# Kernel optimization log

Measured on AMD Instinct MI355X. Metric: run time of the kernel, lower is better.

The kernel has to match this reference:

```python
import jax, jax.numpy as jnp
import numpy as np

B, N, DIM = 4, 2048, 1024
HEAD = 16
INTER = 1024
HD = INTER // HEAD  # 64
SCALE = INTER ** (-0.5)


def setup_inputs() -> dict:
    key = jax.random.key(0)
    k1, k2, k3 = jax.random.split(key, 3)
    features = jax.random.normal(k1, (B, N, DIM), dtype=jnp.float32)
    W_qkv = jax.random.normal(k2, (DIM, 3 * INTER), dtype=jnp.float32) * (DIM ** -0.5)
    W_out = jax.random.normal(k3, (INTER, DIM), dtype=jnp.float32) * (INTER ** -0.5)
    return {"features": features, "W_qkv": W_qkv, "W_out": W_out}


def reference(features, W_qkv, W_out):
    # fc_qkv: [b, n, 3*inter], chunk into q, k, v
    qkv = jnp.einsum('bnd,de->bne', features, W_qkv)
    q, k, v = jnp.split(qkv, 3, axis=-1)
    # b n (h d) -> b n h d
    q = q.reshape(B, N, HEAD, HD)
    k = k.reshape(B, N, HEAD, HD)
    v = v.reshape(B, N, HEAD, HD)
    # scores: b h i j  (scale = inter_dim ** -0.5, as in source)
    alpha = jnp.einsum('bihd,bjhd->bhij', q, k) * SCALE
    att = jax.nn.softmax(alpha, axis=-1)
    out = jnp.einsum('bhij,bjhd->bihd', att, v)
    out = out.reshape(B, N, INTER)
    # fc_out (dropout_ratio=0.0 -> identity)
    return jnp.einsum('bni,id->bnd', out, W_out)
```

## Files before the change

kernel.cpp:

```cpp
#include <hip/hip_runtime.h>
#include <stdint.h>

#define BB 4
#define SEQ 2048
#define DMODEL 1024
#define NHEAD 16
#define HDIM 64
#define INTER 1024
#define QSCALE 0.045084220027780106f

#if __has_builtin(__builtin_amdgcn_exp2f)
#define EXP2F(x) __builtin_amdgcn_exp2f(x)
#else
#define EXP2F(x) exp2f(x)
#endif

typedef unsigned short u16;
typedef __attribute__((ext_vector_type(4))) unsigned short u16x4;
typedef __attribute__((ext_vector_type(4))) short s16x4;
typedef __attribute__((ext_vector_type(8))) short s16x8;
typedef __attribute__((ext_vector_type(4))) float f32x4;
typedef __attribute__((ext_vector_type(16))) float f32x16;

__device__ __forceinline__ u16 f2bf(float f) {
  unsigned int u = __float_as_uint(f);
  u += 0x7FFFu + ((u >> 16) & 1u);
  return (u16)(u >> 16);
}

#if __has_builtin(__builtin_amdgcn_cvt_pk_bf16_f32)
typedef __attribute__((ext_vector_type(2))) __bf16 bf16x2_t;
__device__ __forceinline__ unsigned int pk2bf(float a, float b) {
  bf16x2_t r = __builtin_amdgcn_cvt_pk_bf16_f32(a, b);
  return *reinterpret_cast<unsigned int*>(&r);
}
#else
__device__ __forceinline__ unsigned int pk2bf(float a, float b) {
  return (unsigned int)f2bf(a) | ((unsigned int)f2bf(b) << 16);
}
#endif

__device__ __forceinline__ void async16(const u16* g, u16* l) {
  __builtin_amdgcn_global_load_lds((__attribute__((address_space(1))) void*)(void*)(g),
                                   (__attribute__((address_space(3))) void*)(l),
                                   16, 0, 0);
}

__global__ __launch_bounds__(256) void prep(
    const float* __restrict__ f, const float* __restrict__ wqkv,
    const float* __restrict__ wout, u16* __restrict__ Xb,
    u16* __restrict__ WqkvT, u16* __restrict__ WoutT) {
  __shared__ float tile[32][33];
  const int bid = blockIdx.x, tid = threadIdx.x;
  if (bid < 8192) {
    int i = (bid * 256 + tid) * 4;
    f32x4 v = *reinterpret_cast<const f32x4*>(f + i);
    uint2 o;
    o.x = pk2bf(v[0], v[1]);
    o.y = pk2bf(v[2], v[3]);
    *reinterpret_cast<uint2*>(Xb + i) = o;
  } else {
    const float* src; u16* dst; int rows, cols, bx, by;
    if (bid < 8192 + 3072) {
      int t = bid - 8192;
      src = wqkv; dst = WqkvT; rows = DMODEL; cols = 3 * INTER;
      bx = t % 96; by = t / 96;
    } else {
      int t = bid - 11264;
      src = wout; dst = WoutT; rows = INTER; cols = DMODEL;
      bx = t & 31; by = t >> 5;
    }
    int c0 = bx * 32, r0 = by * 32, tx = tid & 31, ty = tid >> 5;
    #pragma unroll
    for (int i = ty; i < 32; i += 8) tile[i][tx] = src[(size_t)(r0 + i) * cols + c0 + tx];
    __syncthreads();
    #pragma unroll
    for (int i = ty; i < 32; i += 8)
      dst[(size_t)(c0 + i) * rows + r0 + tx] = f2bf(tile[tx][i]);
  }
}

template <int MODE>
__global__ __launch_bounds__(256, 2) void gemm_bt(
    const u16* __restrict__ A, const u16* __restrict__ BT,
    float* __restrict__ Cf, u16* __restrict__ Qb, u16* __restrict__ Kp,
    u16* __restrict__ Vp, int K, int ldc) {
  __shared__ u16 As[128 * 32];
  __shared__ u16 Bs[128 * 32];
  const int tid = threadIdx.x;
  const int wave = tid >> 6, lane = tid & 63;
  const int row0 = blockIdx.y * 128, col0 = blockIdx.x * 128;
  const int wr = (wave >> 1) * 64, wc = (wave & 1) * 64;
  const int r = lane & 15, q8 = (lane >> 4) * 8;

  f32x4 acc[4][4] = {};

  const int sRow = lane >> 2, sK = (lane & 3) * 8;
  const u16* Ag0 = A + (size_t)(row0 + wave * 32 + sRow) * K + sK;
  const u16* Ag1 = Ag0 + (size_t)16 * K;
  const u16* Bg0 = BT + (size_t)(col0 + wave * 32 + sRow) * K + sK;
  const u16* Bg1 = Bg0 + (size_t)16 * K;
  u16* Al0 = &As[wave * 1024];
  u16* Al1 = Al0 + 512;
  u16* Bl0 = &Bs[wave * 1024];
  u16* Bl1 = Bl0 + 512;

  for (int k0 = 0; k0 < K; k0 += 32) {
    async16(Ag0 + k0, Al0);
    async16(Ag1 + k0, Al1);
    async16(Bg0 + k0, Bl0);
    async16(Bg1 + k0, Bl1);
    __syncthreads();
    s16x8 af[4], bf[4];
    #pragma unroll
    for (int t = 0; t < 4; t++) {
      af[t] = *reinterpret_cast<const s16x8*>(&As[(wr + t * 16 + r) * 32 + q8]);
      bf[t] = *reinterpret_cast<const s16x8*>(&Bs[(wc + t * 16 + r) * 32 + q8]);
    }
    #pragma unroll
    for (int i = 0; i < 4; i++)
      #pragma unroll
      for (int j = 0; j < 4; j++)
        acc[i][j] = __builtin_amdgcn_mfma_f32_16x16x32_bf16(af[i], bf[j], acc[i][j], 0, 0, 0);
    __syncthreads();
  }

  const int quad = lane >> 4;
  #pragma unroll
  for (int i = 0; i < 4; i++) {
    const int n = row0 + wr + i * 16 + quad * 4;
    const int b = n >> 11, nn = n & (SEQ - 1);
    #pragma unroll
    for (int j = 0; j < 4; j++) {
      const int gc = col0 + wc + j * 16 + r;
      if (MODE == 1) {
        #pragma unroll
        for (int reg = 0; reg < 4; reg++)
          Cf[(size_t)(n + reg) * ldc + gc] = acc[i][j][reg];
      } else if (gc < INTER) {
        size_t base = (size_t)n * INTER + gc;
        #pragma unroll
        for (int reg = 0; reg < 4; reg++)
          Qb[base + (size_t)reg * INTER] = f2bf(acc[i][j][reg] * QSCALE);
      } else if (gc < 2 * INTER) {
        int dim = gc - INTER, h = dim >> 6, d = dim & 63;
        int bh = b * NHEAD + h;
        size_t base = (((size_t)(bh * 64 + (nn >> 5)) * 4 + (d >> 4)) * 64 +
                       ((((d >> 3) & 1) << 5) | (nn & 31))) * 8 + (d & 7);
        #pragma unroll
        for (int reg = 0; reg < 4; reg++)
          Kp[base + reg * 8] = f2bf(acc[i][j][reg]);
      } else {
        int dim = gc - 2 * INTER, h = dim >> 6, d = dim & 63;
        int bh = b * NHEAD + h;
        size_t base = ((((size_t)(bh * 64 + (nn >> 5)) * 2 + ((nn >> 4) & 1)) * 2 +
                        (d >> 5)) * 64 +
                       ((((nn >> 3) & 1) << 5) | (d & 31))) * 8 + (nn & 7);
        uint2 pk;
        pk.x = pk2bf(acc[i][j][0], acc[i][j][1]);
        pk.y = pk2bf(acc[i][j][2], acc[i][j][3]);
        *reinterpret_cast<uint2*>(Vp + base) = pk;
      }
    }
  }
}

#define ATTN_STEP(JCUR, KC, KN)                                                   \
  {                                                                               \
    const int jnext = ((JCUR) + 1) & 63;                                          \
    _Pragma("unroll")                                                             \
    for (int c = 0; c < 4; c++)                                                   \
      KN[c] = *reinterpret_cast<const s16x8*>(kpb + jnext * 2048 + c * 512);      \
    s16x8 vf[4];                                                                  \
    _Pragma("unroll")                                                             \
    for (int c = 0; c < 4; c++)                                                   \
      vf[c] = *reinterpret_cast<const s16x8*>(vpb + (JCUR) * 2048 + c * 512);     \
    f32x16 st = {};                                                               \
    _Pragma("unroll")                                                             \
    for (int c = 0; c < 4; c++)                                                   \
      st = __builtin_amdgcn_mfma_f32_32x32x16_bf16(KC[c], qf[c], st, 0, 0, 0);    \
    _Pragma("unroll")                                                             \
    for (int q = 0; q < 4; q++) {                                                 \
      float p0 = EXP2F(st[q * 4 + 0]), p1 = EXP2F(st[q * 4 + 1]);                 \
      float p2 = EXP2F(st[q * 4 + 2]), p3 = EXP2F(st[q * 4 + 3]);                 \
      ls += (p0 + p1) + (p2 + p3);                                                \
      uint2 pk;                                                                   \
      pk.x = pk2bf(p0, p1);                                                       \
      pk.y = pk2bf(p2, p3);                                                       \
      *reinterpret_cast<uint2*>(&Pw[l31 * 36 + q * 8 + half * 4]) = pk;           \
    }                                                                             \
    _Pragma("unroll")                                                             \
    for (int kc = 0; kc < 2; kc++) {                                              \
      const u16* pp = &Pw[l31 * 36 + half * 8 + kc * 16];                         \
      s16x4 plo = *reinterpret_cast<const s16x4*>(pp);                            \
      s16x4 phi = *reinterpret_cast<const s16x4*>(pp + 4);                        \
      s16x8 pb = __builtin_shufflevector(plo, phi, 0, 1, 2, 3, 4, 5, 6, 7);       \
      ot0 = __builtin_amdgcn_mfma_f32_32x32x16_bf16(vf[kc * 2 + 0], pb, ot0, 0, 0, 0); \
      ot1 = __builtin_amdgcn_mfma_f32_32x32x16_bf16(vf[kc * 2 + 1], pb, ot1, 0, 0, 0); \
    }                                                                             \
  }

__global__ __launch_bounds__(128, 4) void attn_kernel(
    const u16* __restrict__ Qb, const u16* __restrict__ Kp,
    const u16* __restrict__ Vp, u16* __restrict__ AO) {
  __shared__ __align__(16) u16 Ps[2][32 * 36];
  const int tid = threadIdx.x;
  const int wave = tid >> 6, lane = tid & 63;
  const int l31 = lane & 31, half = lane >> 5;
  const int bh = blockIdx.x, b = bh >> 4, h = bh & 15;
  const int i0 = blockIdx.y * 64 + wave * 32;

  const u16* qbase = Qb + (size_t)(b * SEQ + i0 + l31) * INTER + h * HDIM + half * 8;
  s16x8 qf[4];
  #pragma unroll
  for (int c = 0; c < 4; c++) qf[c] = *reinterpret_cast<const s16x8*>(qbase + c * 16);

  const u16* kpb = Kp + (size_t)bh * (64 * 4 * 512) + lane * 8;
  const u16* vpb = Vp + (size_t)bh * (64 * 4 * 512) + lane * 8;
  u16* Pw = &Ps[wave][0];

  f32x16 ot0 = {}, ot1 = {};
  float ls = 0.f;

  s16x8 kf0[4], kf1[4];
  #pragma unroll
  for (int c = 0; c < 4; c++)
    kf0[c] = *reinterpret_cast<const s16x8*>(kpb + c * 512);

  for (int jb = 0; jb < 64; jb += 2) {
    ATTN_STEP(jb, kf0, kf1)
    ATTN_STEP(jb + 1, kf1, kf0)
  }

  ls += __shfl_xor(ls, 32, 64);
  float rinv = 1.0f / ls;

  u16* orow = AO + (size_t)(b * SEQ + i0 + l31) * INTER + h * HDIM;
  #pragma unroll
  for (int dt = 0; dt < 2; dt++) {
    const f32x16& o = dt ? ot1 : ot0;
    #pragma unroll
    for (int q = 0; q < 4; q++) {
      uint2 pk;
      pk.x = pk2bf(o[q * 4 + 0] * rinv, o[q * 4 + 1] * rinv);
      pk.y = pk2bf(o[q * 4 + 2] * rinv, o[q * 4 + 3] * rinv);
      *reinterpret_cast<uint2*>(orow + dt * 32 + q * 8 + half * 4) = pk;
    }
  }
}

extern "C" void kernel_launch(void* const* d_in, const int* in_sizes, int n_in,
                              void* d_out, int out_size, void* d_ws, size_t ws_size,
                              hipStream_t stream) {
  const float* features = (const float*)d_in[0];
  const float* W_qkv    = (const float*)d_in[1];
  const float* W_out    = (const float*)d_in[2];
  float* out = (float*)d_out;
  char* w = (char*)d_ws;
  u16* Xb    = (u16*)(w);
  u16* WqkvT = (u16*)(w + 16777216);
  u16* WoutT = (u16*)(w + 23068672);
  u16* Qb    = (u16*)(w + 25165824);
  u16* Kp    = (u16*)(w + 41943040);
  u16* Vp    = (u16*)(w + 58720256);
  u16* AO    = (u16*)(w + 75497472);

  prep<<<dim3(12288), dim3(256), 0, stream>>>(features, W_qkv, W_out, Xb, WqkvT, WoutT);
  gemm_bt<0><<<dim3(24, 64), dim3(256), 0, stream>>>(Xb, WqkvT, nullptr, Qb, Kp, Vp,
                                                     DMODEL, 0);
  attn_kernel<<<dim3(64, 32), dim3(128), 0, stream>>>(Qb, Kp, Vp, AO);
  gemm_bt<1><<<dim3(8, 64), dim3(256), 0, stream>>>(AO, WoutT, out, nullptr, nullptr,
                                                    nullptr, INTER, DMODEL);
}
```

Measured before the change: 287.9 us.

## Replace LDS P transpose with permlane32 swaps, add MFMA priority and XCD-aware block mapping

```diff
diff --git a/kernel.cpp b/kernel.cpp
--- a/kernel.cpp
+++ b/kernel.cpp
@@ -21,6 +21,7 @@
 typedef __attribute__((ext_vector_type(8))) short s16x8;
 typedef __attribute__((ext_vector_type(4))) float f32x4;
 typedef __attribute__((ext_vector_type(16))) float f32x16;
+typedef __attribute__((ext_vector_type(4))) unsigned int u32x4;
 
 __device__ __forceinline__ u16 f2bf(float f) {
   unsigned int u = __float_as_uint(f);
@@ -44,6 +45,30 @@
   __builtin_amdgcn_global_load_lds((__attribute__((address_space(1))) void*)(void*)(g),
                                    (__attribute__((address_space(3))) void*)(l),
                                    16, 0, 0);
+}
+
+__device__ __forceinline__ void make_pb(const unsigned int* cc, int half,
+                                        s16x8& pb0, s16x8& pb1) {
+#if __has_builtin(__builtin_amdgcn_permlane32_swap)
+  (void)half;
+  auto r02 = __builtin_amdgcn_permlane32_swap(cc[0], cc[2], false, false);
+  auto r13 = __builtin_amdgcn_permlane32_swap(cc[1], cc[3], false, false);
+  auto r46 = __builtin_amdgcn_permlane32_swap(cc[4], cc[6], false, false);
+  auto r57 = __builtin_amdgcn_permlane32_swap(cc[5], cc[7], false, false);
+  u32x4 w0 = {(unsigned)r02[0], (unsigned)r13[0], (unsigned)r02[1], (unsigned)r13[1]};
+  u32x4 w1 = {(unsigned)r46[0], (unsigned)r57[0], (unsigned)r46[1], (unsigned)r57[1]};
+#else
+  unsigned x0 = __shfl_xor((int)cc[0], 32, 64), x1 = __shfl_xor((int)cc[1], 32, 64);
+  unsigned x2 = __shfl_xor((int)cc[2], 32, 64), x3 = __shfl_xor((int)cc[3], 32, 64);
+  unsigned x4 = __shfl_xor((int)cc[4], 32, 64), x5 = __shfl_xor((int)cc[5], 32, 64);
+  unsigned x6 = __shfl_xor((int)cc[6], 32, 64), x7 = __shfl_xor((int)cc[7], 32, 64);
+  u32x4 w0 = {half ? x2 : cc[0], half ? x3 : cc[1],
+              half ? cc[2] : x0, half ? cc[3] : x1};
+  u32x4 w1 = {half ? x6 : cc[4], half ? x7 : cc[5],
+              half ? cc[6] : x4, half ? cc[7] : x5};
+#endif
+  pb0 = *reinterpret_cast<s16x8*>(&w0);
+  pb1 = *reinterpret_cast<s16x8*>(&w1);
 }
 
 __global__ __launch_bounds__(256) void prep(
@@ -176,39 +201,42 @@
     for (int c = 0; c < 4; c++)                                                   \
       vf[c] = *reinterpret_cast<const s16x8*>(vpb + (JCUR) * 2048 + c * 512);     \
     f32x16 st = {};                                                               \
+    __builtin_amdgcn_s_setprio(1);                                                \
     _Pragma("unroll")                                                             \
     for (int c = 0; c < 4; c++)                                                   \
       st = __builtin_amdgcn_mfma_f32_32x32x16_bf16(KC[c], qf[c], st, 0, 0, 0);    \
+    __builtin_amdgcn_s_setprio(0);                                                \
+    unsigned int cc[8];                                                           \
     _Pragma("unroll")                                                             \
     for (int q = 0; q < 4; q++) {                                                 \
       float p0 = EXP2F(st[q * 4 + 0]), p1 = EXP2F(st[q * 4 + 1]);                 \
       float p2 = EXP2F(st[q * 4 + 2]), p3 = EXP2F(st[q * 4 + 3]);                 \
       ls += (p0 + p1) + (p2 + p3);                                                \
-      uint2 pk;                                                                   \
-      pk.x = pk2bf(p0, p1);                                                       \
-      pk.y = pk2bf(p2, p3);                                                       \
-      *reinterpret_cast<uint2*>(&Pw[l31 * 36 + q * 8 + half * 4]) = pk;           \
+      cc[q * 2 + 0] = pk2bf(p0, p1);                                              \
+      cc[q * 2 + 1] = pk2bf(p2, p3);                                              \
     }                                                                             \
-    _Pragma("unroll")                                                             \
-    for (int kc = 0; kc < 2; kc++) {                                              \
-      const u16* pp = &Pw[l31 * 36 + half * 8 + kc * 16];                         \
-      s16x4 plo = *reinterpret_cast<const s16x4*>(pp);                            \
-      s16x4 phi = *reinterpret_cast<const s16x4*>(pp + 4);                        \
-      s16x8 pb = __builtin_shufflevector(plo, phi, 0, 1, 2, 3, 4, 5, 6, 7);       \
-      ot0 = __builtin_amdgcn_mfma_f32_32x32x16_bf16(vf[kc * 2 + 0], pb, ot0, 0, 0, 0); \
-      ot1 = __builtin_amdgcn_mfma_f32_32x32x16_bf16(vf[kc * 2 + 1], pb, ot1, 0, 0, 0); \
-    }                                                                             \
+    s16x8 pb0, pb1;                                                               \
+    make_pb(cc, half, pb0, pb1);                                                  \
+    __builtin_amdgcn_s_setprio(1);                                                \
+    ot0 = __builtin_amdgcn_mfma_f32_32x32x16_bf16(vf[0], pb0, ot0, 0, 0, 0);      \
+    ot1 = __builtin_amdgcn_mfma_f32_32x32x16_bf16(vf[1], pb0, ot1, 0, 0, 0);      \
+    ot0 = __builtin_amdgcn_mfma_f32_32x32x16_bf16(vf[2], pb1, ot0, 0, 0, 0);      \
+    ot1 = __builtin_amdgcn_mfma_f32_32x32x16_bf16(vf[3], pb1, ot1, 0, 0, 0);      \
+    __builtin_amdgcn_s_setprio(0);                                                \
   }
 
 __global__ __launch_bounds__(128, 4) void attn_kernel(
     const u16* __restrict__ Qb, const u16* __restrict__ Kp,
     const u16* __restrict__ Vp, u16* __restrict__ AO) {
-  __shared__ __align__(16) u16 Ps[2][32 * 36];
   const int tid = threadIdx.x;
   const int wave = tid >> 6, lane = tid & 63;
   const int l31 = lane & 31, half = lane >> 5;
-  const int bh = blockIdx.x, b = bh >> 4, h = bh & 15;
-  const int i0 = blockIdx.y * 64 + wave * 32;
+  const int wg = blockIdx.x;
+  const int xcd = wg & 7, li = wg >> 3;
+  const int bh = xcd + ((li >> 5) << 3);
+  const int iblk = li & 31;
+  const int b = bh >> 4, h = bh & 15;
+  const int i0 = iblk * 64 + wave * 32;
 
   const u16* qbase = Qb + (size_t)(b * SEQ + i0 + l31) * INTER + h * HDIM + half * 8;
   s16x8 qf[4];
@@ -217,7 +245,6 @@
 
   const u16* kpb = Kp + (size_t)bh * (64 * 4 * 512) + lane * 8;
   const u16* vpb = Vp + (size_t)bh * (64 * 4 * 512) + lane * 8;
-  u16* Pw = &Ps[wave][0];
 
   f32x16 ot0 = {}, ot1 = {};
   float ls = 0.f;
@@ -268,7 +295,7 @@
   prep<<<dim3(12288), dim3(256), 0, stream>>>(features, W_qkv, W_out, Xb, WqkvT, WoutT);
   gemm_bt<0><<<dim3(24, 64), dim3(256), 0, stream>>>(Xb, WqkvT, nullptr, Qb, Kp, Vp,
                                                      DMODEL, 0);
-  attn_kernel<<<dim3(64, 32), dim3(128), 0, stream>>>(Qb, Kp, Vp, AO);
+  attn_kernel<<<dim3(64 * 32), dim3(128), 0, stream>>>(Qb, Kp, Vp, AO);
   gemm_bt<1><<<dim3(8, 64), dim3(256), 0, stream>>>(AO, WoutT, out, nullptr, nullptr,
                                                     nullptr, INTER, DMODEL);
 }
```

After: 315.7 us. 9.7% more time.
